# Kernel optimization log

Hardware: AMD Instinct MI355X
Metric: run time of the kernel (lower is better)

The kernel has to match this reference:

```python
import jax, jax.numpy as jnp
import numpy as np

B, Q, R, D = 32, 512, 1024, 2048
L = Q + R
GAMMA, LMBDA, KL_COEFF = 0.99, 0.95, 0.1
PENALISE_NO_EOS = True
REWARD_PENALTY = -3.0
MIN_RESPONSE_LEN = 0
MAX_RESPONSE_LEN = 1024


def setup_inputs() -> dict:
    key = jax.random.key(0)
    k = jax.random.split(key, 6)
    hidden = jax.random.normal(k[0], (B, L, D), jnp.float32)
    w_base = jax.random.normal(k[1], (D,), jnp.float32) / np.float32(np.sqrt(D))
    w_adapter = jax.random.normal(k[2], (D,), jnp.float32) / np.float32(np.sqrt(D))
    gen_logprobs = jax.random.normal(k[3], (B, R), jnp.float32)
    ref_logprobs = jax.random.normal(k[4], (B, R), jnp.float32)
    # left-aligned responses: resp_lens real tokens then padding (True = pad).
    resp_lens = jax.random.randint(k[5], (B,), 1, R + 1)
    responses_pad_mask = jnp.arange(R)[None, :] >= resp_lens[:, None]
    return {"hidden": hidden, "w_base": w_base, "w_adapter": w_adapter,
            "gen_logprobs": gen_logprobs, "ref_logprobs": ref_logprobs,
            "responses_pad_mask": responses_pad_mask, "queries_len": Q}


def _gae(values, rewards):
    # backward-in-time GAE recurrence via lax.scan (reverse=True), vectorized over batch
    v_next = jnp.concatenate([values[:, 1:], jnp.zeros_like(values[:, :1])], axis=1)
    def step(carry, xs):
        v_t, r_t, vn_t = xs
        adv = r_t + GAMMA * vn_t - v_t + GAMMA * LMBDA * carry
        return adv, adv
    init = jnp.zeros(values.shape[0], values.dtype)
    _, advs = jax.lax.scan(step, init, (values.T, rewards.T, v_next.T), reverse=True)
    return advs.T  # [B, R]


def _masked_whiten(x, mask):
    # torchtune masked_whiten: masked mean/var (Bessel-corrected) over all masked entries
    m = mask.astype(x.dtype)
    n = jnp.sum(m)
    mean = jnp.sum(x * m) / n
    var = jnp.sum(((x - mean) ** 2) * m) / n
    var = var * (n / (n - 1.0))  # unbiased
    return (x - mean) * jax.lax.rsqrt(var + 1e-8)


def _forward(hidden, w_base, w_adapter, gen_logprobs, ref_logprobs,
             responses_pad_mask, queries_len):
    b = hidden.shape[0]
    # scorer with adapter -> values; scorer with adapter disabled -> scores
    values_full = jnp.einsum('bld,d->bl', hidden, w_base + w_adapter)
    scores_full = jnp.einsum('bld,d->bl', hidden, w_base)
    values = values_full[:, queries_len - 1:-1]  # [B, R]

    # index of last unmasked (non-pad) response token; 0 if fully padded
    response_last_pos = jnp.argmax(jnp.cumsum(~responses_pad_mask, axis=-1), axis=-1)

    scores = jnp.take_along_axis(
        scores_full, (response_last_pos + queries_len)[:, None], axis=1)[:, 0]

    penalty_mask = jnp.zeros((b,), bool)
    if PENALISE_NO_EOS:
        penalty_mask = penalty_mask | ~jnp.any(responses_pad_mask, axis=-1)
    if MIN_RESPONSE_LEN:
        penalty_mask = penalty_mask | (response_last_pos < MIN_RESPONSE_LEN)
    scores = jnp.where(penalty_mask, jnp.asarray(REWARD_PENALTY, scores.dtype), scores)

    value_last_pos = jnp.where(
        (response_last_pos > 0) & (response_last_pos < MAX_RESPONSE_LEN - 1),
        response_last_pos + 1, response_last_pos)
    value_pad_mask = responses_pad_mask.at[jnp.arange(b), value_last_pos].set(False)
    values = jnp.where(value_pad_mask, jnp.asarray(0.0, values.dtype), values)

    # get_rewards_ppo
    kl = gen_logprobs - ref_logprobs
    kl_rewards = -KL_COEFF * kl
    rewards = kl_rewards.at[jnp.arange(b), value_last_pos].add(scores)

    # estimate_advantages
    advantages = _gae(values, rewards)
    returns = advantages + values
    mask = ~responses_pad_mask
    advantages = jnp.where(mask, _masked_whiten(advantages, mask),
                           jnp.asarray(0.0, advantages.dtype))

    return (values, value_pad_mask, value_last_pos, scores, response_last_pos,
            kl, kl_rewards, advantages, returns)


def reference(hidden, w_base, w_adapter, gen_logprobs, ref_logprobs,
              responses_pad_mask, queries_len):
    return _forward(hidden, w_base, w_adapter, gen_logprobs, ref_logprobs,
                    responses_pad_mask, queries_len)
```

## Files before the change

### kernel.cpp

```cpp
#include <hip/hip_runtime.h>

#define B_   32
#define Q_   512
#define R_   1024
#define D_   2048
#define L_   1536
#define NROW (B_ * 1025)

#define O_VALUES 0
#define O_VPM    32768
#define O_VLP    65536
#define O_SC     65568
#define O_RLP    65600
#define O_KL     65632
#define O_KLR    98400
#define O_ADV    131168
#define O_RET    163936

#define M_FLAG 0
#define M_RLP  1
#define M_VLP  33
#define M_PAD  65
#define M_LIM  97

__global__ __launch_bounds__(1024) void k_prep(
    const void* __restrict__ maskraw,
    int* __restrict__ meta)
{
    __shared__ int sflag;
    const int tid = threadIdx.x;
    if (tid == 0) sflag = 0;
    __syncthreads();

    const unsigned int* mu = (const unsigned int*)maskraw;
    bool odd = false;
    for (int j = tid; j < (B_ * R_) / 4; j += 1024)
        odd |= (mu[j] & 0xFFFFFF00u) != 0u;
    if (odd) atomicOr(&sflag, 1);
    __syncthreads();
    const int byteMode = sflag;

    const int w = tid >> 6, lane = tid & 63;
    for (int p = 0; p < 2; ++p) {
        const int b = w + 16 * p;
        const int base = b * R_ + lane * 16;
        int  ll   = -1;
        bool anyT = false;
        if (byteMode) {
            const unsigned char* mb = (const unsigned char*)maskraw;
#pragma unroll
            for (int j = 0; j < 16; ++j) {
                const bool m = mb[base + j] != 0;
                if (!m) ll = lane * 16 + j;
                anyT |= m;
            }
        } else {
            const int* mi = (const int*)maskraw;
#pragma unroll
            for (int j = 0; j < 16; ++j) {
                const bool m = mi[base + j] != 0;
                if (!m) ll = lane * 16 + j;
                anyT |= m;
            }
        }
#pragma unroll
        for (int d = 1; d < 64; d <<= 1) {
            int o = __shfl_xor(ll, d, 64);
            ll = ll > o ? ll : o;
        }
        const int  rlp    = ll < 0 ? 0 : ll;
        const bool anyPad = (__ballot(anyT) != 0ull);
        const int  vlp    = (rlp > 0 && rlp < R_ - 1) ? rlp + 1 : rlp;
        if (lane == 0) {
            meta[M_RLP + b] = rlp;
            meta[M_VLP + b] = vlp;
            meta[M_PAD + b] = anyPad ? 1 : 0;
            meta[M_LIM + b] = rlp + 1;
        }
    }
    if (tid == 0) meta[M_FLAG] = byteMode;
}

__global__ __launch_bounds__(256) void k_dots(
    const float* __restrict__ hidden,
    const float* __restrict__ wb,
    const float* __restrict__ wa,
    const int*   __restrict__ meta,
    float* __restrict__ vals_dot,
    float* __restrict__ scores_dot)
{
    const int lane = threadIdx.x & 63;
    const int wid  = blockIdx.x * 4 + (threadIdx.x >> 6);
    const int nw   = gridDim.x * 4;

    const float4* wb4 = (const float4*)wb;
    const float4* wa4 = (const float4*)wa;
    float4 vb[8], vs[8];
#pragma unroll
    for (int k = 0; k < 8; ++k) {
        float4 bv = wb4[lane + 64 * k];
        float4 av = wa4[lane + 64 * k];
        vb[k] = bv;
        vs[k] = make_float4(bv.x + av.x, bv.y + av.y, bv.z + av.z, bv.w + av.w);
    }

    for (int row = wid; row < NROW; row += nw) {
        const int bb = row / 1025;
        const int i  = row - bb * 1025;
        if (i > meta[M_LIM + bb]) continue;
        const float4* hp =
            (const float4*)(hidden + ((size_t)bb * L_ + 511 + i) * (size_t)D_);
        float4 h[8];
#pragma unroll
        for (int k = 0; k < 8; ++k) h[k] = hp[lane + 64 * k];
        float db = 0.f, ds = 0.f;
#pragma unroll
        for (int k = 0; k < 8; ++k) {
            db += h[k].x * vb[k].x + h[k].y * vb[k].y + h[k].z * vb[k].z + h[k].w * vb[k].w;
            ds += h[k].x * vs[k].x + h[k].y * vs[k].y + h[k].z * vs[k].z + h[k].w * vs[k].w;
        }
#pragma unroll
        for (int d = 32; d > 0; d >>= 1) {
            db += __shfl_down(db, d, 64);
            ds += __shfl_down(ds, d, 64);
        }
        if (lane == 0) { vals_dot[row] = ds; scores_dot[row] = db; }
    }
}

__global__ __launch_bounds__(1024) void k_seq2(
    const float* __restrict__ vals_dot,
    const float* __restrict__ scores_dot,
    const float* __restrict__ gen,
    const float* __restrict__ ref,
    const void*  __restrict__ maskraw,
    const int*   __restrict__ meta,
    float* __restrict__ out)
{
    __shared__ double red0[16], red1[16], red2[16];
    __shared__ float  smean, srs;

    const int tid  = threadIdx.x;
    const int w    = tid >> 6, lane = tid & 63;
    const int byteMode = meta[M_FLAG];

    const float c  = 0.99f * 0.95f;
    const float c2 = c * c, c4 = c2 * c2, c8 = c4 * c4, c16 = c8 * c8;

    float        aP[2][16];
    unsigned int pm[2];
    double sx = 0.0, sx2 = 0.0, nn = 0.0;

    for (int p = 0; p < 2; ++p) {
        const int b      = w + 16 * p;
        const int rlp    = meta[M_RLP + b];
        const int vlp    = meta[M_VLP + b];
        const int anyPad = meta[M_PAD + b];
        const int base   = b * R_ + lane * 16;

        unsigned int mbits = 0;
        if (byteMode) {
            const unsigned char* mb = (const unsigned char*)maskraw;
#pragma unroll
            for (int j = 0; j < 16; ++j) mbits |= (mb[base + j] ? 1u : 0u) << j;
        } else {
            const int* mi = (const int*)maskraw;
#pragma unroll
            for (int j = 0; j < 16; ++j) mbits |= (mi[base + j] ? 1u : 0u) << j;
        }
        pm[p] = mbits;

        const float score = anyPad ? scores_dot[b * 1025 + rlp + 1] : -3.0f;

        float v[16], dl[16];
#pragma unroll
        for (int j = 0; j < 16; ++j) {
            const int  t   = lane * 16 + j;
            const bool mj  = (mbits >> j) & 1u;
            const bool vpm = mj && (t != vlp);
            const float vv = vpm ? 0.f : vals_dot[b * 1025 + t];
            v[j] = vv;
            out[O_VALUES + b * R_ + t] = vv;
            out[O_VPM + b * R_ + t]    = vpm ? 1.f : 0.f;
        }
        float tsh = __shfl_down(v[0], 1, 64);
        const float vnh = (lane == 63) ? 0.f : tsh;

#pragma unroll
        for (int j = 0; j < 16; ++j) {
            const int t = lane * 16 + j;
            const float kl = gen[b * R_ + t] - ref[b * R_ + t];
            out[O_KL + b * R_ + t] = kl;
            const float klr = -0.1f * kl;
            out[O_KLR + b * R_ + t] = klr;
            const float rw = klr + ((t == vlp) ? score : 0.f);
            const float vn = (j < 15) ? v[j + 1] : vnh;
            dl[j] = rw + 0.99f * vn - v[j];
        }

        float a[16];
        a[15] = dl[15];
#pragma unroll
        for (int j = 14; j >= 0; --j) a[j] = dl[j] + c * a[j + 1];

        float S = a[0], f = c16;
#pragma unroll
        for (int d = 1; d < 64; d <<= 1) {
            float up = __shfl_down(S, d, 64);
            up = (lane + d < 64) ? up : 0.f;
            S += f * up;
            f *= f;
        }
        float t1 = __shfl_down(S, 1, 64);
        float carry = (lane == 63) ? 0.f : t1;
#pragma unroll
        for (int j = 15; j >= 0; --j) { a[j] = dl[j] + c * carry; carry = a[j]; }

#pragma unroll
        for (int j = 0; j < 16; ++j) {
            const int t = lane * 16 + j;
            out[O_RET + b * R_ + t] = a[j] + v[j];
            aP[p][j] = a[j];
            if (!((mbits >> j) & 1u)) {
                sx  += (double)a[j];
                sx2 += (double)a[j] * (double)a[j];
                nn  += 1.0;
            }
        }
        if (lane == 0) {
            out[O_VLP + b] = (float)vlp;
            out[O_SC + b]  = score;
            out[O_RLP + b] = (float)rlp;
        }
    }

#pragma unroll
    for (int d = 1; d < 64; d <<= 1) {
        sx  += __shfl_xor(sx, d, 64);
        sx2 += __shfl_xor(sx2, d, 64);
        nn  += __shfl_xor(nn, d, 64);
    }
    if (lane == 0) { red0[w] = sx; red1[w] = sx2; red2[w] = nn; }
    __syncthreads();
    if (tid == 0) {
        double SX = 0.0, SX2 = 0.0, N = 0.0;
        for (int i = 0; i < 16; ++i) { SX += red0[i]; SX2 += red1[i]; N += red2[i]; }
        const double mean = SX / N;
        const double var  = (SX2 - SX * SX / N) / (N - 1.0);
        smean = (float)mean;
        srs   = (float)(1.0 / sqrt(var + 1e-8));
    }
    __syncthreads();
    const float mean = smean, rsc = srs;

    for (int p = 0; p < 2; ++p) {
        const int b = w + 16 * p;
#pragma unroll
        for (int j = 0; j < 16; ++j) {
            const int t = lane * 16 + j;
            const bool mj = (pm[p] >> j) & 1u;
            out[O_ADV + b * R_ + t] = mj ? 0.f : (aP[p][j] - mean) * rsc;
        }
    }
}

extern "C" void kernel_launch(void* const* d_in, const int* in_sizes, int n_in,
                              void* d_out, int out_size, void* d_ws, size_t ws_size,
                              hipStream_t stream) {
    const float* hidden = (const float*)d_in[0];
    const float* wb     = (const float*)d_in[1];
    const float* wa     = (const float*)d_in[2];
    const float* gen    = (const float*)d_in[3];
    const float* ref    = (const float*)d_in[4];
    const void*  mask   = d_in[5];

    float* out = (float*)d_out;
    float* wsf = (float*)d_ws;
    float* vals_dot   = wsf;
    float* scores_dot = wsf + NROW;
    int*   meta       = (int*)((char*)d_ws + (size_t)2 * NROW * sizeof(float));

    hipLaunchKernelGGL(k_prep, dim3(1), dim3(1024), 0, stream, mask, meta);
    hipLaunchKernelGGL(k_dots, dim3(2048), dim3(256), 0, stream,
                       hidden, wb, wa, meta, vals_dot, scores_dot);
    hipLaunchKernelGGL(k_seq2, dim3(1), dim3(1024), 0, stream,
                       vals_dot, scores_dot, gen, ref, mask, meta, out);
}
```

Baseline: 564.0 us.

## Split GAE across batch blocks with atomic stats and separate whitening kernel

The single-block GAE/whitening kernel becomes one 64-thread block per batch row. The per-row sums go into global double atomics, and a new grid-wide kernel applies the whitening afterwards. The dot-product kernel now gives each batch row a fixed group of 256 waves that loop only up to that row's limit, which removes the per-row divide and branch. This spreads the serial tail across more compute units, at the cost of an extra memset, an extra kernel launch, and an extra pass over the advantages. The fixed work assignment also risks load imbalance across rows of different lengths.

```diff
diff --git a/kernel.cpp b/kernel.cpp
--- a/kernel.cpp
+++ b/kernel.cpp
@@ -91,7 +91,10 @@
 {
     const int lane = threadIdx.x & 63;
     const int wid  = blockIdx.x * 4 + (threadIdx.x >> 6);
-    const int nw   = gridDim.x * 4;
+    const int bb   = wid >> 8;
+    const int widx = wid & 255;
+
+    const int lim = meta[M_LIM + bb];
 
     const float4* wb4 = (const float4*)wb;
     const float4* wa4 = (const float4*)wa;
@@ -104,10 +107,7 @@
         vs[k] = make_float4(bv.x + av.x, bv.y + av.y, bv.z + av.z, bv.w + av.w);
     }
 
-    for (int row = wid; row < NROW; row += nw) {
-        const int bb = row / 1025;
-        const int i  = row - bb * 1025;
-        if (i > meta[M_LIM + bb]) continue;
+    for (int i = widx; i <= lim; i += 256) {
         const float4* hp =
             (const float4*)(hidden + ((size_t)bb * L_ + 511 + i) * (size_t)D_);
         float4 h[8];
@@ -124,144 +124,137 @@
             db += __shfl_down(db, d, 64);
             ds += __shfl_down(ds, d, 64);
         }
-        if (lane == 0) { vals_dot[row] = ds; scores_dot[row] = db; }
-    }
-}
-
-__global__ __launch_bounds__(1024) void k_seq2(
+        if (lane == 0) {
+            const int row = bb * 1025 + i;
+            vals_dot[row] = ds;
+            scores_dot[row] = db;
+        }
+    }
+}
+
+__global__ __launch_bounds__(64) void k_seq(
     const float* __restrict__ vals_dot,
     const float* __restrict__ scores_dot,
     const float* __restrict__ gen,
     const float* __restrict__ ref,
     const void*  __restrict__ maskraw,
     const int*   __restrict__ meta,
-    float* __restrict__ out)
-{
-    __shared__ double red0[16], red1[16], red2[16];
-    __shared__ float  smean, srs;
-
-    const int tid  = threadIdx.x;
-    const int w    = tid >> 6, lane = tid & 63;
+    float* __restrict__ out,
+    double* __restrict__ acc)
+{
+    const int b    = blockIdx.x;
+    const int lane = threadIdx.x;
     const int byteMode = meta[M_FLAG];
-
-    const float c  = 0.99f * 0.95f;
+    const int rlp    = meta[M_RLP + b];
+    const int vlp    = meta[M_VLP + b];
+    const int anyPad = meta[M_PAD + b];
+
+    const int base = b * R_ + lane * 16;
+    unsigned int mbits = 0;
+    if (byteMode) {
+        const unsigned char* mb = (const unsigned char*)maskraw;
+#pragma unroll
+        for (int j = 0; j < 16; ++j) mbits |= (mb[base + j] ? 1u : 0u) << j;
+    } else {
+        const int* mi = (const int*)maskraw;
+#pragma unroll
+        for (int j = 0; j < 16; ++j) mbits |= (mi[base + j] ? 1u : 0u) << j;
+    }
+
+    const float score = anyPad ? scores_dot[b * 1025 + rlp + 1] : -3.0f;
+
+    float v[16];
+#pragma unroll
+    for (int j = 0; j < 16; ++j) {
+        const int  t   = lane * 16 + j;
+        const bool mj  = (mbits >> j) & 1u;
+        const bool vpm = mj && (t != vlp);
+        const float vv = vpm ? 0.f : vals_dot[b * 1025 + t];
+        v[j] = vv;
+        out[O_VALUES + b * R_ + t] = vv;
+        out[O_VPM + b * R_ + t]    = vpm ? 1.f : 0.f;
+    }
+    float tsh = __shfl_down(v[0], 1, 64);
+    const float vnh = (lane == 63) ? 0.f : tsh;
+
+    const float c = 0.99f * 0.95f;
+    float dl[16];
+#pragma unroll
+    for (int j = 0; j < 16; ++j) {
+        const int t = lane * 16 + j;
+        const float kl = gen[b * R_ + t] - ref[b * R_ + t];
+        out[O_KL + b * R_ + t]  = kl;
+        const float klr = -0.1f * kl;
+        out[O_KLR + b * R_ + t] = klr;
+        const float rw = klr + ((t == vlp) ? score : 0.f);
+        const float vn = (j < 15) ? v[j + 1] : vnh;
+        dl[j] = rw + 0.99f * vn - v[j];
+    }
+
+    float a[16];
+    a[15] = dl[15];
+#pragma unroll
+    for (int j = 14; j >= 0; --j) a[j] = dl[j] + c * a[j + 1];
+
     const float c2 = c * c, c4 = c2 * c2, c8 = c4 * c4, c16 = c8 * c8;
-
-    float        aP[2][16];
-    unsigned int pm[2];
+    float S = a[0], f = c16;
+#pragma unroll
+    for (int d = 1; d < 64; d <<= 1) {
+        float up = __shfl_down(S, d, 64);
+        up = (lane + d < 64) ? up : 0.f;
+        S += f * up;
+        f *= f;
+    }
+    float t1 = __shfl_down(S, 1, 64);
+    float carry = (lane == 63) ? 0.f : t1;
+#pragma unroll
+    for (int j = 15; j >= 0; --j) { a[j] = dl[j] + c * carry; carry = a[j]; }
+
     double sx = 0.0, sx2 = 0.0, nn = 0.0;
-
-    for (int p = 0; p < 2; ++p) {
-        const int b      = w + 16 * p;
-        const int rlp    = meta[M_RLP + b];
-        const int vlp    = meta[M_VLP + b];
-        const int anyPad = meta[M_PAD + b];
-        const int base   = b * R_ + lane * 16;
-
-        unsigned int mbits = 0;
-        if (byteMode) {
-            const unsigned char* mb = (const unsigned char*)maskraw;
-#pragma unroll
-            for (int j = 0; j < 16; ++j) mbits |= (mb[base + j] ? 1u : 0u) << j;
-        } else {
-            const int* mi = (const int*)maskraw;
-#pragma unroll
-            for (int j = 0; j < 16; ++j) mbits |= (mi[base + j] ? 1u : 0u) << j;
-        }
-        pm[p] = mbits;
-
-        const float score = anyPad ? scores_dot[b * 1025 + rlp + 1] : -3.0f;
-
-        float v[16], dl[16];
-#pragma unroll
-        for (int j = 0; j < 16; ++j) {
-            const int  t   = lane * 16 + j;
-            const bool mj  = (mbits >> j) & 1u;
-            const bool vpm = mj && (t != vlp);
-            const float vv = vpm ? 0.f : vals_dot[b * 1025 + t];
-            v[j] = vv;
-            out[O_VALUES + b * R_ + t] = vv;
-            out[O_VPM + b * R_ + t]    = vpm ? 1.f : 0.f;
-        }
-        float tsh = __shfl_down(v[0], 1, 64);
-        const float vnh = (lane == 63) ? 0.f : tsh;
-
-#pragma unroll
-        for (int j = 0; j < 16; ++j) {
-            const int t = lane * 16 + j;
-            const float kl = gen[b * R_ + t] - ref[b * R_ + t];
-            out[O_KL + b * R_ + t] = kl;
-            const float klr = -0.1f * kl;
-            out[O_KLR + b * R_ + t] = klr;
-            const float rw = klr + ((t == vlp) ? score : 0.f);
-            const float vn = (j < 15) ? v[j + 1] : vnh;
-            dl[j] = rw + 0.99f * vn - v[j];
-        }
-
-        float a[16];
-        a[15] = dl[15];
-#pragma unroll
-        for (int j = 14; j >= 0; --j) a[j] = dl[j] + c * a[j + 1];
-
-        float S = a[0], f = c16;
-#pragma unroll
-        for (int d = 1; d < 64; d <<= 1) {
-            float up = __shfl_down(S, d, 64);
-            up = (lane + d < 64) ? up : 0.f;
-            S += f * up;
-            f *= f;
-        }
-        float t1 = __shfl_down(S, 1, 64);
-        float carry = (lane == 63) ? 0.f : t1;
-#pragma unroll
-        for (int j = 15; j >= 0; --j) { a[j] = dl[j] + c * carry; carry = a[j]; }
-
-#pragma unroll
-        for (int j = 0; j < 16; ++j) {
-            const int t = lane * 16 + j;
-            out[O_RET + b * R_ + t] = a[j] + v[j];
-            aP[p][j] = a[j];
-            if (!((mbits >> j) & 1u)) {
-                sx  += (double)a[j];
-                sx2 += (double)a[j] * (double)a[j];
-                nn  += 1.0;
-            }
-        }
-        if (lane == 0) {
-            out[O_VLP + b] = (float)vlp;
-            out[O_SC + b]  = score;
-            out[O_RLP + b] = (float)rlp;
-        }
-    }
-
+#pragma unroll
+    for (int j = 0; j < 16; ++j) {
+        const int t = lane * 16 + j;
+        out[O_ADV + b * R_ + t] = a[j];
+        out[O_RET + b * R_ + t] = a[j] + v[j];
+        if (!((mbits >> j) & 1u)) {
+            sx  += (double)a[j];
+            sx2 += (double)a[j] * (double)a[j];
+            nn  += 1.0;
+        }
+    }
 #pragma unroll
     for (int d = 1; d < 64; d <<= 1) {
         sx  += __shfl_xor(sx, d, 64);
         sx2 += __shfl_xor(sx2, d, 64);
         nn  += __shfl_xor(nn, d, 64);
     }
-    if (lane == 0) { red0[w] = sx; red1[w] = sx2; red2[w] = nn; }
-    __syncthreads();
-    if (tid == 0) {
-        double SX = 0.0, SX2 = 0.0, N = 0.0;
-        for (int i = 0; i < 16; ++i) { SX += red0[i]; SX2 += red1[i]; N += red2[i]; }
-        const double mean = SX / N;
-        const double var  = (SX2 - SX * SX / N) / (N - 1.0);
-        smean = (float)mean;
-        srs   = (float)(1.0 / sqrt(var + 1e-8));
-    }
-    __syncthreads();
-    const float mean = smean, rsc = srs;
-
-    for (int p = 0; p < 2; ++p) {
-        const int b = w + 16 * p;
-#pragma unroll
-        for (int j = 0; j < 16; ++j) {
-            const int t = lane * 16 + j;
-            const bool mj = (pm[p] >> j) & 1u;
-            out[O_ADV + b * R_ + t] = mj ? 0.f : (aP[p][j] - mean) * rsc;
-        }
-    }
+    if (lane == 0) {
+        atomicAdd(&acc[0], sx);
+        atomicAdd(&acc[1], sx2);
+        atomicAdd(&acc[2], nn);
+        out[O_VLP + b] = (float)vlp;
+        out[O_SC + b]  = score;
+        out[O_RLP + b] = (float)rlp;
+    }
+}
+
+__global__ __launch_bounds__(256) void k_whiten(
+    float* __restrict__ out,
+    const double* __restrict__ acc,
+    const void* __restrict__ maskraw,
+    const int* __restrict__ meta)
+{
+    const int i = blockIdx.x * blockDim.x + threadIdx.x;
+    if (i >= B_ * R_) return;
+    const double sx = acc[0], sx2 = acc[1], n = acc[2];
+    const double mean = sx / n;
+    const double var  = (sx2 - sx * sx / n) / (n - 1.0);
+    const float  rs   = (float)(1.0 / sqrt(var + 1e-8));
+    bool pad;
+    if (meta[M_FLAG]) pad = ((const unsigned char*)maskraw)[i] != 0;
+    else              pad = ((const int*)maskraw)[i] != 0;
+    const float x = out[O_ADV + i];
+    out[O_ADV + i] = pad ? 0.f : (x - (float)mean) * rs;
 }
 
 extern "C" void kernel_launch(void* const* d_in, const int* in_sizes, int n_in,
@@ -278,11 +271,15 @@
     float* wsf = (float*)d_ws;
     float* vals_dot   = wsf;
     float* scores_dot = wsf + NROW;
-    int*   meta       = (int*)((char*)d_ws + (size_t)2 * NROW * sizeof(float));
-
+    int*    meta = (int*)((char*)d_ws + (size_t)2 * NROW * sizeof(float));
+    double* acc  = (double*)((char*)d_ws + (size_t)2 * NROW * sizeof(float) + 512);
+
+    hipMemsetAsync(acc, 0, 3 * sizeof(double), stream);
     hipLaunchKernelGGL(k_prep, dim3(1), dim3(1024), 0, stream, mask, meta);
     hipLaunchKernelGGL(k_dots, dim3(2048), dim3(256), 0, stream,
                        hidden, wb, wa, meta, vals_dot, scores_dot);
-    hipLaunchKernelGGL(k_seq2, dim3(1), dim3(1024), 0, stream,
-                       vals_dot, scores_dot, gen, ref, mask, meta, out);
-}
+    hipLaunchKernelGGL(k_seq, dim3(B_), dim3(64), 0, stream,
+                       vals_dot, scores_dot, gen, ref, mask, meta, out, acc);
+    hipLaunchKernelGGL(k_whiten, dim3((B_ * R_ + 255) / 256), dim3(256), 0, stream,
+                       out, acc, mask, meta);
+}
```

Measured after the change: 492.4 us. 12.7% less time.
